# Optimization experiments

Measured on AMD Instinct MI355X. Metric: run time of the kernel, lower is better.

## Reference

```python
import jax, jax.numpy as jnp
import numpy as np

N_NODES = 100000
TIME_LEN = 128
OUT_CH = 5          # temp_out_dim
KERNEL = 7
STRIDE = 3
CONV_OUT_LEN = (TIME_LEN - KERNEL) // STRIDE + 1  # 41
EMB = 32            # temp_emb_dim
HID = EMB // 2      # 16
N_EDGES = 3200000


def setup_inputs() -> dict:
    key = jax.random.key(0)
    ks = jax.random.split(key, 16)
    x = jax.random.normal(ks[0], (N_NODES, TIME_LEN), dtype=jnp.float32)
    edge_index = jax.random.randint(ks[1], (2, N_EDGES), 0, N_NODES, dtype=jnp.int64)
    s = 0.05
    return {
        "x": x,
        "edge_index": edge_index,
        "conv_w": jax.random.normal(ks[2], (OUT_CH, 1, KERNEL), dtype=jnp.float32) * s,
        "conv_b": jax.random.normal(ks[3], (OUT_CH,), dtype=jnp.float32) * s,
        "fc_w": jax.random.normal(ks[4], (EMB, OUT_CH * CONV_OUT_LEN), dtype=jnp.float32) * s,
        "fc_b": jax.random.normal(ks[5], (EMB,), dtype=jnp.float32) * s,
        "g1w1": jax.random.normal(ks[6], (HID, EMB), dtype=jnp.float32) * s,
        "g1b1": jax.random.normal(ks[7], (HID,), dtype=jnp.float32) * s,
        "g1w2": jax.random.normal(ks[8], (HID, HID), dtype=jnp.float32) * s,
        "g1b2": jax.random.normal(ks[9], (HID,), dtype=jnp.float32) * s,
        "g2w1": jax.random.normal(ks[10], (HID, HID), dtype=jnp.float32) * s,
        "g2b1": jax.random.normal(ks[11], (HID,), dtype=jnp.float32) * s,
        "g2w2": jax.random.normal(ks[12], (HID, HID), dtype=jnp.float32) * s,
        "g2b2": jax.random.normal(ks[13], (HID,), dtype=jnp.float32) * s,
        "ro_w": jax.random.normal(ks[14], (1, HID), dtype=jnp.float32) * s,
        "ro_b": jax.random.normal(ks[15], (1,), dtype=jnp.float32) * s,
    }


def _gin_conv(h, edge_index, w1, b1, w2, b2):
    # sum-aggregate neighbor features into target nodes (eps = 0)
    agg = jax.ops.segment_sum(h[edge_index[0]], edge_index[1], num_segments=N_NODES)
    z = h + agg
    # MLP: Linear -> ReLU -> Linear
    return jax.nn.relu(z @ w1.T + b1) @ w2.T + b2


def reference(x, edge_index, conv_w, conv_b, fc_w, fc_b,
              g1w1, g1b1, g1w2, g1b2, g2w1, g2b1, g2w2, g2b2, ro_w, ro_b):
    n = x.shape[0]
    # temporal Conv1d: [N,1,T] -> [N,OUT_CH,CONV_OUT_LEN]
    h = jax.lax.conv_general_dilated(
        x[:, None, :], conv_w, window_strides=(STRIDE,), padding='VALID',
        dimension_numbers=('NCH', 'OIH', 'NCH'))
    h = jax.nn.relu(h + conv_b[None, :, None])
    h = h.reshape(n, -1)                 # channel-major flatten, matches torch .view
    h = h @ fc_w.T + fc_b                # [N, EMB]
    # GIN layer 1 (+ ReLU between layers)
    h = jax.nn.relu(_gin_conv(h, edge_index, g1w1, g1b1, g1w2, g1b2))
    # GIN layer 2 (no activation after final layer)
    h = _gin_conv(h, edge_index, g2w1, g2b1, g2w2, g2b2)
    return h @ ro_w.T + ro_b             # [N, 1]
```

## Files before the change

kernel.cpp:

```cpp
#include <hip/hip_runtime.h>

#define NN   100000
#define TL   128
#define OC   5
#define KW   7
#define ST   3
#define CL   41
#define FLAT 205
#define EMB  32
#define HID  16
#define NE   3200000

#define CLP  44
#define JP   220
#define JB   55
#define WN   8
#define SXW  1048

#define BBUCK  391
#define NPB    14336
#define TILE   4096
#define NBIN   782
#define CNODES 64
#define NGB    1563
#define NS     2560
#define SENT   0xFFFFFFFFu

__device__ __forceinline__ void f4add(float4& a, const float4 v) {
    a.x += v.x; a.y += v.y; a.z += v.z; a.w += v.w;
}

__global__ __launch_bounds__(256) void k_prep(
    const float* __restrict__ g1w1, const float* __restrict__ fc_w,
    const float* __restrict__ fc_b,
    float* __restrict__ wcTl, float* __restrict__ bc,
    int* __restrict__ gcur)
{
    int tid = threadIdx.x;
    for (int idx = tid; idx < HID * JP; idx += 256) {
        int l  = idx / JP;
        int jp = idx - l * JP;
        int c  = jp / CLP;
        int t  = jp - c * CLP;
        float s = 0.f;
        if (t < CL) {
            int j = c * CL + t;
            #pragma unroll
            for (int m = 0; m < EMB; ++m)
                s = fmaf(g1w1[l * EMB + m], fc_w[m * FLAT + j], s);
        }
        wcTl[idx] = s;
    }
    if (tid < HID) {
        float s = 0.f;
        #pragma unroll
        for (int m = 0; m < EMB; ++m)
            s = fmaf(g1w1[tid * EMB + m], fc_b[m], s);
        bc[tid] = s;
    }
    for (int b = tid; b < BBUCK; b += 256)
        gcur[b] = b * NPB;
}

__global__ __launch_bounds__(256) void k_convfc(
    const float* __restrict__ x,
    const float* __restrict__ conv_w, const float* __restrict__ conv_b,
    const float* __restrict__ wcTl,  const float* __restrict__ bc,
    float* __restrict__ p1)
{
    __shared__ float s_x[4 * SXW];
    __shared__ float s_h2[4 * WN * JP];
    const int tid  = threadIdx.x;
    const int wv   = tid >> 6;
    const int lane = tid & 63;
    const long long nw = (long long)blockIdx.x * 32 + wv * WN;

    float* sx = s_x  + wv * SXW;
    float* sh = s_h2 + wv * (WN * JP);

    const float4* xv = (const float4*)(x + nw * TL);
    #pragma unroll
    for (int c = 0; c < 4; ++c) {
        int f4  = c * 64 + lane;
        int row = f4 >> 5;
        int c4  = f4 & 31;
        float4 v = xv[f4];
        float* d = sx + row * 129 + c4 * 4;
        d[0] = v.x; d[1] = v.y; d[2] = v.z; d[3] = v.w;
    }
    asm volatile("s_waitcnt lgkmcnt(0)" ::: "memory");

    for (int i = lane; i < 55 * WN; i += 64) {
        int n  = i & (WN - 1);
        int ci = i >> 3;
        int c  = ci / 11;
        int tg = ci - c * 11;
        int t0 = tg * 4;
        const float* xr = sx + n * 129 + t0 * ST;
        float xx[16];
        #pragma unroll
        for (int k = 0; k < 16; ++k) xx[k] = xr[k];
        const float* wr = conv_w + c * KW;
        float w0 = wr[0], w1 = wr[1], w2 = wr[2], w3 = wr[3],
              w4 = wr[4], w5 = wr[5], w6 = wr[6];
        float bb = conv_b[c];
        float4 r;
        r.x = fmaxf(bb + xx[0]*w0 + xx[1]*w1 + xx[2]*w2 + xx[3]*w3
                       + xx[4]*w4 + xx[5]*w5 + xx[6]*w6, 0.f);
        r.y = (t0 + 1 < CL)
            ? fmaxf(bb + xx[3]*w0 + xx[4]*w1 + xx[5]*w2 + xx[6]*w3
                       + xx[7]*w4 + xx[8]*w5 + xx[9]*w6, 0.f) : 0.f;
        r.z = (t0 + 2 < CL)
            ? fmaxf(bb + xx[6]*w0 + xx[7]*w1 + xx[8]*w2 + xx[9]*w3
                       + xx[10]*w4 + xx[11]*w5 + xx[12]*w6, 0.f) : 0.f;
        r.w = (t0 + 3 < CL)
            ? fmaxf(bb + xx[9]*w0 + xx[10]*w1 + xx[11]*w2 + xx[12]*w3
                       + xx[13]*w4 + xx[14]*w5 + xx[15]*w6, 0.f) : 0.f;
        *(float4*)(sh + n * JP + c * CLP + t0) = r;
    }
    asm volatile("s_waitcnt lgkmcnt(0)" ::: "memory");

    const int l = lane & 15;
    const int g = lane >> 4;
    float a0 = bc[l];
    float a1 = a0;
    const float4* wl = (const float4*)(wcTl + l * JP);
    const float4* h0 = (const float4*)(sh + g * JP);
    const float4* h1 = (const float4*)(sh + (g + 4) * JP);
    #pragma unroll 5
    for (int jb = 0; jb < JB; ++jb) {
        float4 w = wl[jb];
        float4 p = h0[jb];
        float4 q = h1[jb];
        a0 = fmaf(p.x, w.x, fmaf(p.y, w.y, fmaf(p.z, w.z, fmaf(p.w, w.w, a0))));
        a1 = fmaf(q.x, w.x, fmaf(q.y, w.y, fmaf(q.z, w.z, fmaf(q.w, w.w, a1))));
    }
    p1[(nw + g)     * HID + l] = a0;
    p1[(nw + g + 4) * HID + l] = a1;
}

__global__ __launch_bounds__(256) void k_bin(
    const int* __restrict__ ei, int* __restrict__ gcur,
    unsigned int* __restrict__ gbin)
{
    __shared__ unsigned int s_stage[TILE];
    __shared__ int s_cnt[BBUCK], s_ofs[BBUCK], s_base[BBUCK];
    __shared__ int s_sum[256];

    const int tid = threadIdx.x;
    const int e0  = blockIdx.x * TILE;
    const int cntE = min(TILE, NE - e0);

    for (int b = tid; b < BBUCK; b += 256) s_cnt[b] = 0;
    __syncthreads();

    for (int i = tid; i < cntE; i += 256)
        atomicAdd(&s_cnt[ei[NE + e0 + i] >> 8], 1);
    __syncthreads();

    for (int b = tid; b < BBUCK; b += 256) {
        int c = s_cnt[b];
        s_base[b] = c ? atomicAdd(&gcur[b], (c + 15) & ~15) : 0;
    }

    int v0 = 0, v1 = 0;
    {
        int i0 = tid * 2;
        if (i0     < BBUCK) v0 = s_cnt[i0];
        if (i0 + 1 < BBUCK) v1 = s_cnt[i0 + 1];
    }
    int csum = v0 + v1;
    s_sum[tid] = csum;
    __syncthreads();
    #pragma unroll
    for (int d = 1; d < 256; d <<= 1) {
        int t = (tid >= d) ? s_sum[tid - d] : 0;
        __syncthreads();
        s_sum[tid] += t;
        __syncthreads();
    }
    {
        int run = s_sum[tid] - csum;
        int i0 = tid * 2;
        if (i0     < BBUCK) { s_ofs[i0]     = run; run += v0; }
        if (i0 + 1 < BBUCK) { s_ofs[i0 + 1] = run; }
    }
    __syncthreads();

    for (int i = tid; i < cntE; i += 256) {
        int s = ei[e0 + i];
        int d = ei[NE + e0 + i];
        int b = d >> 8;
        int pos = atomicAdd(&s_ofs[b], 1);
        s_stage[pos] = ((unsigned int)(d & 255) << 17) | (unsigned int)s;
    }
    __syncthreads();

    const int wid = tid >> 6, lane = tid & 63;
    for (int b = wid; b < BBUCK; b += 4) {
        int cnt = s_cnt[b];
        if (!cnt) continue;
        int res = (cnt + 15) & ~15;
        int rdo = s_ofs[b] - cnt;
        int gb  = s_base[b];
        int lim = min(res, b * NPB + NPB - gb);
        for (int j = lane; j < lim; j += 64)
            gbin[(size_t)gb + j] = (j < cnt) ? s_stage[rdo + j] : SENT;
    }
}

__global__ __launch_bounds__(256) void k_sort(
    const unsigned int* __restrict__ gbin, const int* __restrict__ gcur,
    int* __restrict__ goff, int* __restrict__ gsorted)
{
    __shared__ unsigned int s_m[NS];
    __shared__ int s_cnt[CNODES], s_ofs[CNODES], s_loc[CNODES];
    __shared__ int s_n;
    const int tid = threadIdx.x;
    const int b64 = blockIdx.x;
    const int bkt = b64 >> 2, q = b64 & 3;
    const int nslots = min(gcur[bkt] - bkt * NPB, NPB);
    const unsigned int* run = gbin + (size_t)bkt * NPB;

    if (tid < CNODES) s_cnt[tid] = 0;
    if (tid == 0) s_n = 0;
    __syncthreads();

    for (int i = tid; i < nslots; i += 256) {
        unsigned int w = run[i];
        if (w != SENT && (int)(w >> 23) == q) {
            int p = atomicAdd(&s_n, 1);
            if (p < NS) {
                s_m[p] = w;
                atomicAdd(&s_cnt[(w >> 17) & 63], 1);
            }
        }
    }
    __syncthreads();

    if (tid < CNODES) s_ofs[tid] = s_cnt[tid];
    __syncthreads();
    #pragma unroll
    for (int d = 1; d < CNODES; d <<= 1) {
        int t = (tid < CNODES && tid >= d) ? s_ofs[tid - d] : 0;
        __syncthreads();
        if (tid < CNODES) s_ofs[tid] += t;
        __syncthreads();
    }
    if (tid < CNODES) {
        int inc = s_ofs[tid];
        s_loc[tid] = inc - s_cnt[tid];
        goff[(size_t)b64 * 65 + tid + 1] = inc;
    }
    if (tid == 0) goff[(size_t)b64 * 65] = 0;
    __syncthreads();

    const int n = min(s_n, NS);
    int* dst = gsorted + (size_t)b64 * NS;
    for (int i = tid; i < n; i += 256) {
        unsigned int w = s_m[i];
        int pos = atomicAdd(&s_loc[(w >> 17) & 63], 1);
        dst[pos] = (int)(w & 0x1FFFFu);
    }
}

__global__ __launch_bounds__(256) void k_gagg1(
    const float* __restrict__ feat, const int* __restrict__ goff,
    const int* __restrict__ gsorted,
    const float* __restrict__ b1, const float* __restrict__ w2,
    const float* __restrict__ b2, const float* __restrict__ w3,
    float* __restrict__ outfeat)
{
    __shared__ float s_acc[CNODES * 16];
    __shared__ float s_w2[HID * HID], s_w3[HID * HID], s_b1[HID], s_b2[HID];
    __shared__ int s_off[CNODES + 1];
    const int tid = threadIdx.x;
    const int b   = blockIdx.x;

    s_w2[tid] = w2[tid];
    s_w3[tid] = w3[tid];
    if (tid < HID) { s_b1[tid] = b1[tid]; s_b2[tid] = b2[tid]; }
    if (tid < CNODES + 1) s_off[tid] = goff[(size_t)b * 65 + tid];
    __syncthreads();

    const int node = tid >> 2, q = tid & 3;
    const int* srcs = gsorted + (size_t)b * NS;
    const float4* pv = (const float4*)feat;
    float4 acc0 = make_float4(0.f, 0.f, 0.f, 0.f);
    float4 acc1 = make_float4(0.f, 0.f, 0.f, 0.f);
    int j = s_off[node];
    const int e = s_off[node + 1];
    for (; j + 7 < e; j += 8) {
        int s0 = srcs[j],     s1 = srcs[j + 1], s2 = srcs[j + 2], s3 = srcs[j + 3];
        int s4 = srcs[j + 4], s5 = srcs[j + 5], s6 = srcs[j + 6], s7 = srcs[j + 7];
        float4 v0 = pv[(size_t)s0 * 4 + q];
        float4 v1 = pv[(size_t)s1 * 4 + q];
        float4 v2 = pv[(size_t)s2 * 4 + q];
        float4 v3 = pv[(size_t)s3 * 4 + q];
        float4 v4 = pv[(size_t)s4 * 4 + q];
        float4 v5 = pv[(size_t)s5 * 4 + q];
        float4 v6 = pv[(size_t)s6 * 4 + q];
        float4 v7 = pv[(size_t)s7 * 4 + q];
        f4add(acc0, v0); f4add(acc1, v1); f4add(acc0, v2); f4add(acc1, v3);
        f4add(acc0, v4); f4add(acc1, v5); f4add(acc0, v6); f4add(acc1, v7);
    }
    for (; j + 3 < e; j += 4) {
        int s0 = srcs[j], s1 = srcs[j + 1], s2 = srcs[j + 2], s3 = srcs[j + 3];
        float4 v0 = pv[(size_t)s0 * 4 + q];
        float4 v1 = pv[(size_t)s1 * 4 + q];
        float4 v2 = pv[(size_t)s2 * 4 + q];
        float4 v3 = pv[(size_t)s3 * 4 + q];
        f4add(acc0, v0); f4add(acc1, v1); f4add(acc0, v2); f4add(acc1, v3);
    }
    for (; j < e; ++j)
        f4add(acc0, pv[(size_t)srcs[j] * 4 + q]);
    f4add(acc0, acc1);
    ((float4*)s_acc)[node * 4 + q] = acc0;
    __syncthreads();

    const int gn = b * CNODES + tid;
    if (tid < CNODES && gn < NN) {
        const float4* fr = (const float4*)(feat + (size_t)gn * HID);
        const float4* sa = (const float4*)(s_acc + tid * 16);
        float t[HID];
        #pragma unroll
        for (int i2 = 0; i2 < 4; ++i2) {
            float4 f = fr[i2], a = sa[i2];
            t[i2*4+0] = fmaxf(f.x + a.x + s_b1[i2*4+0], 0.f);
            t[i2*4+1] = fmaxf(f.y + a.y + s_b1[i2*4+1], 0.f);
            t[i2*4+2] = fmaxf(f.z + a.z + s_b1[i2*4+2], 0.f);
            t[i2*4+3] = fmaxf(f.w + a.w + s_b1[i2*4+3], 0.f);
        }
        float h[HID];
        #pragma unroll
        for (int i2 = 0; i2 < HID; ++i2) {
            float acc = s_b2[i2];
            #pragma unroll
            for (int jj = 0; jj < HID; ++jj) acc += t[jj] * s_w2[i2 * HID + jj];
            h[i2] = fmaxf(acc, 0.f);
        }
        float o[HID];
        #pragma unroll
        for (int i2 = 0; i2 < HID; ++i2) {
            float acc = 0.f;
            #pragma unroll
            for (int jj = 0; jj < HID; ++jj) acc += h[jj] * s_w3[i2 * HID + jj];
            o[i2] = acc;
        }
        float4* po = (float4*)(outfeat + (size_t)gn * HID);
        #pragma unroll
        for (int i2 = 0; i2 < 4; ++i2)
            po[i2] = make_float4(o[i2*4+0], o[i2*4+1], o[i2*4+2], o[i2*4+3]);
    }
}

__global__ __launch_bounds__(256) void k_gagg2(
    const float* __restrict__ feat, const int* __restrict__ goff,
    const int* __restrict__ gsorted,
    const float* __restrict__ b1, const float* __restrict__ w2,
    const float* __restrict__ b2, const float* __restrict__ row,
    const float* __restrict__ rob,
    float* __restrict__ out)
{
    __shared__ float s_acc[CNODES * 16];
    __shared__ float s_w2[HID * HID], s_b1[HID], s_b2[HID], s_ro[HID];
    __shared__ int s_off[CNODES + 1];
    const int tid = threadIdx.x;
    const int b   = blockIdx.x;

    s_w2[tid] = w2[tid];
    if (tid < HID) { s_b1[tid] = b1[tid]; s_b2[tid] = b2[tid]; s_ro[tid] = row[tid]; }
    if (tid < CNODES + 1) s_off[tid] = goff[(size_t)b * 65 + tid];
    __syncthreads();

    const int node = tid >> 2, q = tid & 3;
    const int* srcs = gsorted + (size_t)b * NS;
    const float4* pv = (const float4*)feat;
    float4 acc0 = make_float4(0.f, 0.f, 0.f, 0.f);
    float4 acc1 = make_float4(0.f, 0.f, 0.f, 0.f);
    int j = s_off[node];
    const int e = s_off[node + 1];
    for (; j + 7 < e; j += 8) {
        int s0 = srcs[j],     s1 = srcs[j + 1], s2 = srcs[j + 2], s3 = srcs[j + 3];
        int s4 = srcs[j + 4], s5 = srcs[j + 5], s6 = srcs[j + 6], s7 = srcs[j + 7];
        float4 v0 = pv[(size_t)s0 * 4 + q];
        float4 v1 = pv[(size_t)s1 * 4 + q];
        float4 v2 = pv[(size_t)s2 * 4 + q];
        float4 v3 = pv[(size_t)s3 * 4 + q];
        float4 v4 = pv[(size_t)s4 * 4 + q];
        float4 v5 = pv[(size_t)s5 * 4 + q];
        float4 v6 = pv[(size_t)s6 * 4 + q];
        float4 v7 = pv[(size_t)s7 * 4 + q];
        f4add(acc0, v0); f4add(acc1, v1); f4add(acc0, v2); f4add(acc1, v3);
        f4add(acc0, v4); f4add(acc1, v5); f4add(acc0, v6); f4add(acc1, v7);
    }
    for (; j + 3 < e; j += 4) {
        int s0 = srcs[j], s1 = srcs[j + 1], s2 = srcs[j + 2], s3 = srcs[j + 3];
        float4 v0 = pv[(size_t)s0 * 4 + q];
        float4 v1 = pv[(size_t)s1 * 4 + q];
        float4 v2 = pv[(size_t)s2 * 4 + q];
        float4 v3 = pv[(size_t)s3 * 4 + q];
        f4add(acc0, v0); f4add(acc1, v1); f4add(acc0, v2); f4add(acc1, v3);
    }
    for (; j < e; ++j)
        f4add(acc0, pv[(size_t)srcs[j] * 4 + q]);
    f4add(acc0, acc1);
    ((float4*)s_acc)[node * 4 + q] = acc0;
    __syncthreads();

    const int gn = b * CNODES + tid;
    if (tid < CNODES && gn < NN) {
        const float4* fr = (const float4*)(feat + (size_t)gn * HID);
        const float4* sa = (const float4*)(s_acc + tid * 16);
        float t[HID];
        #pragma unroll
        for (int i2 = 0; i2 < 4; ++i2) {
            float4 f = fr[i2], a = sa[i2];
            t[i2*4+0] = fmaxf(f.x + a.x + s_b1[i2*4+0], 0.f);
            t[i2*4+1] = fmaxf(f.y + a.y + s_b1[i2*4+1], 0.f);
            t[i2*4+2] = fmaxf(f.z + a.z + s_b1[i2*4+2], 0.f);
            t[i2*4+3] = fmaxf(f.w + a.w + s_b1[i2*4+3], 0.f);
        }
        float res = rob[0];
        #pragma unroll
        for (int i2 = 0; i2 < HID; ++i2) {
            float acc = s_b2[i2];
            #pragma unroll
            for (int jj = 0; jj < HID; ++jj) acc += t[jj] * s_w2[i2 * HID + jj];
            res += acc * s_ro[i2];
        }
        out[gn] = res;
    }
}

__global__ __launch_bounds__(256) void k_embed(
    const float* __restrict__ x,
    const float* __restrict__ conv_w, const float* __restrict__ conv_b,
    const float* __restrict__ fc_w,   const float* __restrict__ fc_b,
    const float* __restrict__ g1w1,
    float* __restrict__ p1)
{
    __shared__ float s_x[4][TL];
    __shared__ float s_h[4][FLAT + 3];
    __shared__ float s_e[4][EMB];

    const int w    = threadIdx.x >> 6;
    const int lane = threadIdx.x & 63;
    const int node = blockIdx.x * 4 + w;

    const float2* xr = (const float2*)(x + (size_t)node * TL);
    float2 v = xr[lane];
    s_x[w][lane * 2 + 0] = v.x;
    s_x[w][lane * 2 + 1] = v.y;
    __syncthreads();

    for (int o = lane; o < FLAT; o += 64) {
        int c = o / CL;
        int t = o - c * CL;
        float acc = conv_b[c];
        #pragma unroll
        for (int k = 0; k < KW; ++k)
            acc += s_x[w][t * ST + k] * conv_w[c * KW + k];
        s_h[w][o] = fmaxf(acc, 0.f);
    }
    __syncthreads();

    if (lane < EMB) {
        float acc = fc_b[lane];
        const float* wr = fc_w + lane * FLAT;
        for (int j = 0; j < FLAT; ++j)
            acc += s_h[w][j] * wr[j];
        s_e[w][lane] = acc;
    }
    __syncthreads();

    if (lane < HID) {
        float acc = 0.f;
        const float* wr = g1w1 + lane * EMB;
        #pragma unroll
        for (int j = 0; j < EMB; ++j)
            acc += s_e[w][j] * wr[j];
        p1[(size_t)node * HID + lane] = acc;
    }
}

__global__ __launch_bounds__(256) void k_scatter(
    const float* __restrict__ p, const int* __restrict__ ei,
    float* __restrict__ agg)
{
    long long t = (long long)blockIdx.x * 256 + threadIdx.x;
    int e = (int)(t >> 4);
    int k = (int)(t & 15);
    if (e >= NE) return;
    int src = ei[e];
    int dst = ei[NE + e];
    float v = p[(size_t)src * HID + k];
    atomicAdd(agg + (size_t)dst * HID + k, v);
}

__global__ __launch_bounds__(256) void k_mlp1(
    const float* __restrict__ p1, const float* __restrict__ agg,
    const float* __restrict__ b1, const float* __restrict__ w2,
    const float* __restrict__ b2, const float* __restrict__ w3,
    float* __restrict__ p2)
{
    __shared__ float s_w2[HID * HID], s_w3[HID * HID], s_b1[HID], s_b2[HID];
    int tid = threadIdx.x;
    s_w2[tid] = w2[tid];
    s_w3[tid] = w3[tid];
    if (tid < HID) { s_b1[tid] = b1[tid]; s_b2[tid] = b2[tid]; }
    __syncthreads();

    int n = blockIdx.x * 256 + tid;
    if (n >= NN) return;

    float t[HID], h[HID];
    const float4* pa = (const float4*)(p1  + (size_t)n * HID);
    const float4* pb = (const float4*)(agg + (size_t)n * HID);
    #pragma unroll
    for (int i = 0; i < 4; ++i) {
        float4 a = pa[i], b = pb[i];
        t[i*4+0] = fmaxf(a.x + b.x + s_b1[i*4+0], 0.f);
        t[i*4+1] = fmaxf(a.y + b.y + s_b1[i*4+1], 0.f);
        t[i*4+2] = fmaxf(a.z + b.z + s_b1[i*4+2], 0.f);
        t[i*4+3] = fmaxf(a.w + b.w + s_b1[i*4+3], 0.f);
    }
    #pragma unroll
    for (int i = 0; i < HID; ++i) {
        float acc = s_b2[i];
        #pragma unroll
        for (int j = 0; j < HID; ++j) acc += t[j] * s_w2[i * HID + j];
        h[i] = fmaxf(acc, 0.f);
    }
    float o[HID];
    #pragma unroll
    for (int i = 0; i < HID; ++i) {
        float acc = 0.f;
        #pragma unroll
        for (int j = 0; j < HID; ++j) acc += h[j] * s_w3[i * HID + j];
        o[i] = acc;
    }
    float4* po = (float4*)(p2 + (size_t)n * HID);
    #pragma unroll
    for (int i = 0; i < 4; ++i)
        po[i] = make_float4(o[i*4+0], o[i*4+1], o[i*4+2], o[i*4+3]);
}

__global__ __launch_bounds__(256) void k_final(
    const float* __restrict__ p2, const float* __restrict__ agg2,
    const float* __restrict__ b1, const float* __restrict__ w2,
    const float* __restrict__ b2, const float* __restrict__ row,
    const float* __restrict__ rob,
    float* __restrict__ out)
{
    __shared__ float s_w2[HID * HID], s_b1[HID], s_b2[HID], s_ro[HID];
    int tid = threadIdx.x;
    s_w2[tid] = w2[tid];
    if (tid < HID) { s_b1[tid] = b1[tid]; s_b2[tid] = b2[tid]; s_ro[tid] = row[tid]; }
    __syncthreads();

    int n = blockIdx.x * 256 + tid;
    if (n >= NN) return;

    float t[HID];
    const float4* pa = (const float4*)(p2   + (size_t)n * HID);
    const float4* pb = (const float4*)(agg2 + (size_t)n * HID);
    #pragma unroll
    for (int i = 0; i < 4; ++i) {
        float4 a = pa[i], b = pb[i];
        t[i*4+0] = fmaxf(a.x + b.x + s_b1[i*4+0], 0.f);
        t[i*4+1] = fmaxf(a.y + b.y + s_b1[i*4+1], 0.f);
        t[i*4+2] = fmaxf(a.z + b.z + s_b1[i*4+2], 0.f);
        t[i*4+3] = fmaxf(a.w + b.w + s_b1[i*4+3], 0.f);
    }
    float res = rob[0];
    #pragma unroll
    for (int i = 0; i < HID; ++i) {
        float acc = s_b2[i];
        #pragma unroll
        for (int j = 0; j < HID; ++j) acc += t[j] * s_w2[i * HID + j];
        res += acc * s_ro[i];
    }
    out[n] = res;
}

extern "C" void kernel_launch(void* const* d_in, const int* in_sizes, int n_in,
                              void* d_out, int out_size, void* d_ws, size_t ws_size,
                              hipStream_t stream)
{
    const float* x      = (const float*)d_in[0];
    const int*   ei     = (const int*)  d_in[1];
    const float* conv_w = (const float*)d_in[2];
    const float* conv_b = (const float*)d_in[3];
    const float* fc_w   = (const float*)d_in[4];
    const float* fc_b   = (const float*)d_in[5];
    const float* g1w1   = (const float*)d_in[6];
    const float* g1b1   = (const float*)d_in[7];
    const float* g1w2   = (const float*)d_in[8];
    const float* g1b2   = (const float*)d_in[9];
    const float* g2w1   = (const float*)d_in[10];
    const float* g2b1   = (const float*)d_in[11];
    const float* g2w2   = (const float*)d_in[12];
    const float* g2b2   = (const float*)d_in[13];
    const float* ro_w   = (const float*)d_in[14];
    const float* ro_b   = (const float*)d_in[15];
    float* out = (float*)d_out;

    float* A    = (float*)d_ws;
    float* B    = A + (size_t)NN * HID;
    float* wcTl = B + (size_t)NN * HID;
    float* bc   = wcTl + (size_t)HID * JP;
    int*   gcur = (int*)(bc + 16);
    unsigned int* gbin = (unsigned int*)(gcur + BBUCK);
    int*   goff    = (int*)(gbin + (size_t)BBUCK * NPB);
    int*   gsorted = goff + (size_t)NGB * 65;
    const size_t need = (size_t)((char*)(gsorted + (size_t)NGB * NS) - (char*)d_ws);

    if (ws_size >= need) {
        k_prep<<<1, 256, 0, stream>>>(g1w1, fc_w, fc_b, wcTl, bc, gcur);
        k_convfc<<<NN / 32, 256, 0, stream>>>(x, conv_w, conv_b, wcTl, bc, A);
        k_bin<<<NBIN, 256, 0, stream>>>(ei, gcur, gbin);
        k_sort<<<NGB, 256, 0, stream>>>(gbin, gcur, goff, gsorted);
        k_gagg1<<<NGB, 256, 0, stream>>>(A, goff, gsorted, g1b1, g1w2, g1b2,
                                         g2w1, B);
        k_gagg2<<<NGB, 256, 0, stream>>>(B, goff, gsorted, g2b1, g2w2, g2b2,
                                         ro_w, ro_b, out);
    } else {
        k_embed<<<NN / 4, 256, 0, stream>>>(x, conv_w, conv_b, fc_w, fc_b,
                                            g1w1, A);
        hipMemsetAsync(B, 0, (size_t)NN * HID * sizeof(float), stream);
        k_scatter<<<(int)(((long long)NE * HID) / 256), 256, 0, stream>>>(A, ei, B);
        k_mlp1<<<(NN + 255) / 256, 256, 0, stream>>>(A, B, g1b1, g1w2, g1b2,
                                                     g2w1, A);
        hipMemsetAsync(B, 0, (size_t)NN * HID * sizeof(float), stream);
        k_scatter<<<(int)(((long long)NE * HID) / 256), 256, 0, stream>>>(A, ei, B);
        k_final<<<(NN + 255) / 256, 256, 0, stream>>>(A, B, g2b1, g2w2, g2b2,
                                                      ro_w, ro_b, out);
    }
}
```

Baseline: 362.4 us.

## Merge conv/FC embedding and edge binning into one heterogeneous kernel launch

Fuses the independent conv+FC embedding kernel and the edge-binning kernel into a single launch where every fifth block does edge binning and the other four do conv/FC work on node tiles. Shared memory becomes one union buffer sized for the larger role. This lets the compute-heavy embedding and the memory/atomic-heavy binning run concurrently on the GPU and removes one launch boundary. The cost is that every block reserves the larger shared-memory footprint, which may lower occupancy, and the interleaved block schedule can cause imbalance.

After: 363.7 us. About the same (+0.4%).

```diff
diff --git a/kernel.cpp b/kernel.cpp
--- a/kernel.cpp
+++ b/kernel.cpp
@@ -16,15 +16,19 @@
 #define JB   55
 #define WN   8
 #define SXW  1048
+#define NCVB 3125
 
 #define BBUCK  391
 #define NPB    14336
 #define TILE   4096
 #define NBIN   782
+#define CVBG   3910
 #define CNODES 64
 #define NGB    1563
 #define NS     2560
 #define SENT   0xFFFFFFFFu
+
+#define SMEMF  11232
 
 __device__ __forceinline__ void f4add(float4& a, const float4 v) {
     a.x += v.x; a.y += v.y; a.z += v.z; a.w += v.w;
@@ -62,18 +66,96 @@
         gcur[b] = b * NPB;
 }
 
-__global__ __launch_bounds__(256) void k_convfc(
+__global__ __launch_bounds__(256) void k_convbin(
     const float* __restrict__ x,
     const float* __restrict__ conv_w, const float* __restrict__ conv_b,
     const float* __restrict__ wcTl,  const float* __restrict__ bc,
-    float* __restrict__ p1)
-{
-    __shared__ float s_x[4 * SXW];
-    __shared__ float s_h2[4 * WN * JP];
-    const int tid  = threadIdx.x;
+    float* __restrict__ p1,
+    const int* __restrict__ ei, int* __restrict__ gcur,
+    unsigned int* __restrict__ gbin)
+{
+    __shared__ float smem[SMEMF];
+    const int bid = blockIdx.x;
+    const int grp = bid / 5, pos = bid - grp * 5;
+    const int tid = threadIdx.x;
+
+    if (pos == 4) {
+        unsigned int* s_stage = (unsigned int*)smem;
+        int* s_cnt  = (int*)smem + TILE;
+        int* s_ofs  = s_cnt  + BBUCK;
+        int* s_base = s_ofs  + BBUCK;
+        int* s_sum  = s_base + BBUCK;
+
+        const int e0   = grp * TILE;
+        const int cntE = min(TILE, NE - e0);
+
+        for (int b = tid; b < BBUCK; b += 256) s_cnt[b] = 0;
+        __syncthreads();
+
+        for (int i = tid; i < cntE; i += 256)
+            atomicAdd(&s_cnt[ei[NE + e0 + i] >> 8], 1);
+        __syncthreads();
+
+        for (int b = tid; b < BBUCK; b += 256) {
+            int c = s_cnt[b];
+            s_base[b] = c ? atomicAdd(&gcur[b], (c + 15) & ~15) : 0;
+        }
+
+        int v0 = 0, v1 = 0;
+        {
+            int i0 = tid * 2;
+            if (i0     < BBUCK) v0 = s_cnt[i0];
+            if (i0 + 1 < BBUCK) v1 = s_cnt[i0 + 1];
+        }
+        int csum = v0 + v1;
+        s_sum[tid] = csum;
+        __syncthreads();
+        #pragma unroll
+        for (int d = 1; d < 256; d <<= 1) {
+            int t = (tid >= d) ? s_sum[tid - d] : 0;
+            __syncthreads();
+            s_sum[tid] += t;
+            __syncthreads();
+        }
+        {
+            int run = s_sum[tid] - csum;
+            int i0 = tid * 2;
+            if (i0     < BBUCK) { s_ofs[i0]     = run; run += v0; }
+            if (i0 + 1 < BBUCK) { s_ofs[i0 + 1] = run; }
+        }
+        __syncthreads();
+
+        for (int i = tid; i < cntE; i += 256) {
+            int s = ei[e0 + i];
+            int d = ei[NE + e0 + i];
+            int b = d >> 8;
+            int pp = atomicAdd(&s_ofs[b], 1);
+            s_stage[pp] = ((unsigned int)(d & 255) << 17) | (unsigned int)s;
+        }
+        __syncthreads();
+
+        const int wid = tid >> 6, lane = tid & 63;
+        for (int b = wid; b < BBUCK; b += 4) {
+            int cnt = s_cnt[b];
+            if (!cnt) continue;
+            int res = (cnt + 15) & ~15;
+            int rdo = s_ofs[b] - cnt;
+            int gb  = s_base[b];
+            int lim = min(res, b * NPB + NPB - gb);
+            for (int j = lane; j < lim; j += 64)
+                gbin[(size_t)gb + j] = (j < cnt) ? s_stage[rdo + j] : SENT;
+        }
+        return;
+    }
+
+    const int cb = grp * 4 + pos;
+    if (cb >= NCVB) return;
+
+    float* s_x  = smem;
+    float* s_h2 = smem + 4 * SXW;
     const int wv   = tid >> 6;
     const int lane = tid & 63;
-    const long long nw = (long long)blockIdx.x * 32 + wv * WN;
+    const long long nw = (long long)cb * 32 + wv * WN;
 
     float* sx = s_x  + wv * SXW;
     float* sh = s_h2 + wv * (WN * JP);
@@ -137,76 +219,6 @@
     }
     p1[(nw + g)     * HID + l] = a0;
     p1[(nw + g + 4) * HID + l] = a1;
-}
-
-__global__ __launch_bounds__(256) void k_bin(
-    const int* __restrict__ ei, int* __restrict__ gcur,
-    unsigned int* __restrict__ gbin)
-{
-    __shared__ unsigned int s_stage[TILE];
-    __shared__ int s_cnt[BBUCK], s_ofs[BBUCK], s_base[BBUCK];
-    __shared__ int s_sum[256];
-
-    const int tid = threadIdx.x;
-    const int e0  = blockIdx.x * TILE;
-    const int cntE = min(TILE, NE - e0);
-
-    for (int b = tid; b < BBUCK; b += 256) s_cnt[b] = 0;
-    __syncthreads();
-
-    for (int i = tid; i < cntE; i += 256)
-        atomicAdd(&s_cnt[ei[NE + e0 + i] >> 8], 1);
-    __syncthreads();
-
-    for (int b = tid; b < BBUCK; b += 256) {
-        int c = s_cnt[b];
-        s_base[b] = c ? atomicAdd(&gcur[b], (c + 15) & ~15) : 0;
-    }
-
-    int v0 = 0, v1 = 0;
-    {
-        int i0 = tid * 2;
-        if (i0     < BBUCK) v0 = s_cnt[i0];
-        if (i0 + 1 < BBUCK) v1 = s_cnt[i0 + 1];
-    }
-    int csum = v0 + v1;
-    s_sum[tid] = csum;
-    __syncthreads();
-    #pragma unroll
-    for (int d = 1; d < 256; d <<= 1) {
-        int t = (tid >= d) ? s_sum[tid - d] : 0;
-        __syncthreads();
-        s_sum[tid] += t;
-        __syncthreads();
-    }
-    {
-        int run = s_sum[tid] - csum;
-        int i0 = tid * 2;
-        if (i0     < BBUCK) { s_ofs[i0]     = run; run += v0; }
-        if (i0 + 1 < BBUCK) { s_ofs[i0 + 1] = run; }
-    }
-    __syncthreads();
-
-    for (int i = tid; i < cntE; i += 256) {
-        int s = ei[e0 + i];
-        int d = ei[NE + e0 + i];
-        int b = d >> 8;
-        int pos = atomicAdd(&s_ofs[b], 1);
-        s_stage[pos] = ((unsigned int)(d & 255) << 17) | (unsigned int)s;
-    }
-    __syncthreads();
-
-    const int wid = tid >> 6, lane = tid & 63;
-    for (int b = wid; b < BBUCK; b += 4) {
-        int cnt = s_cnt[b];
-        if (!cnt) continue;
-        int res = (cnt + 15) & ~15;
-        int rdo = s_ofs[b] - cnt;
-        int gb  = s_base[b];
-        int lim = min(res, b * NPB + NPB - gb);
-        for (int j = lane; j < lim; j += 64)
-            gbin[(size_t)gb + j] = (j < cnt) ? s_stage[rdo + j] : SENT;
-    }
 }
 
 __global__ __launch_bounds__(256) void k_sort(
@@ -618,8 +630,8 @@
 
     if (ws_size >= need) {
         k_prep<<<1, 256, 0, stream>>>(g1w1, fc_w, fc_b, wcTl, bc, gcur);
-        k_convfc<<<NN / 32, 256, 0, stream>>>(x, conv_w, conv_b, wcTl, bc, A);
-        k_bin<<<NBIN, 256, 0, stream>>>(ei, gcur, gbin);
+        k_convbin<<<CVBG, 256, 0, stream>>>(x, conv_w, conv_b, wcTl, bc, A,
+                                            ei, gcur, gbin);
         k_sort<<<NGB, 256, 0, stream>>>(gbin, gcur, goff, gsorted);
         k_gagg1<<<NGB, 256, 0, stream>>>(A, goff, gsorted, g1b1, g1w2, g1b2,
                                          g2w1, B);
```

## Fuse per-block edge sort into first GIN aggregation kernel; parallelize prep

Applied to the files above, without the earlier changes.

Merges the counting-sort kernel with the first GIN aggregation. The sorted source indices stay in shared memory and are read from there during the gather, while still being written to global memory for the second layer. This removes one kernel launch and a global round trip of the sorted indices and offsets. Separately, the weight-folding prep kernel now runs on 8 blocks instead of 1. Shared memory per block grows (an extra 2560-int array), which may lower occupancy for the latency-bound gather.

New measurement: 349.8 us. 3.5% less time.

```diff
diff --git a/kernel.cpp b/kernel.cpp
--- a/kernel.cpp
+++ b/kernel.cpp
@@ -36,8 +36,9 @@
     float* __restrict__ wcTl, float* __restrict__ bc,
     int* __restrict__ gcur)
 {
-    int tid = threadIdx.x;
-    for (int idx = tid; idx < HID * JP; idx += 256) {
+    const int gid = blockIdx.x * 256 + threadIdx.x;
+    const int gs  = gridDim.x * 256;
+    for (int idx = gid; idx < HID * JP; idx += gs) {
         int l  = idx / JP;
         int jp = idx - l * JP;
         int c  = jp / CLP;
@@ -51,14 +52,14 @@
         }
         wcTl[idx] = s;
     }
-    if (tid < HID) {
+    if (gid < HID) {
         float s = 0.f;
         #pragma unroll
         for (int m = 0; m < EMB; ++m)
-            s = fmaf(g1w1[tid * EMB + m], fc_b[m], s);
-        bc[tid] = s;
-    }
-    for (int b = tid; b < BBUCK; b += 256)
+            s = fmaf(g1w1[gid * EMB + m], fc_b[m], s);
+        bc[gid] = s;
+    }
+    for (int b = gid; b < BBUCK; b += gs)
         gcur[b] = b * NPB;
 }
 
@@ -209,26 +210,37 @@
     }
 }
 
-__global__ __launch_bounds__(256) void k_sort(
+__global__ __launch_bounds__(256) void k_sgagg1(
     const unsigned int* __restrict__ gbin, const int* __restrict__ gcur,
-    int* __restrict__ goff, int* __restrict__ gsorted)
+    const float* __restrict__ feat,
+    const float* __restrict__ b1, const float* __restrict__ w2,
+    const float* __restrict__ b2, const float* __restrict__ w3,
+    int* __restrict__ goff, int* __restrict__ gsorted,
+    float* __restrict__ outfeat)
 {
     __shared__ unsigned int s_m[NS];
-    __shared__ int s_cnt[CNODES], s_ofs[CNODES], s_loc[CNODES];
+    __shared__ int s_sorted[NS];
+    __shared__ float s_acc[CNODES * 16];
+    __shared__ float s_w2[HID * HID], s_w3[HID * HID], s_b1[HID], s_b2[HID];
+    __shared__ int s_cnt[CNODES], s_scan[CNODES], s_loc[CNODES];
+    __shared__ int s_ofx[CNODES + 1];
     __shared__ int s_n;
     const int tid = threadIdx.x;
     const int b64 = blockIdx.x;
-    const int bkt = b64 >> 2, q = b64 & 3;
+    const int bkt = b64 >> 2, qp = b64 & 3;
     const int nslots = min(gcur[bkt] - bkt * NPB, NPB);
     const unsigned int* run = gbin + (size_t)bkt * NPB;
 
+    s_w2[tid] = w2[tid];
+    s_w3[tid] = w3[tid];
+    if (tid < HID) { s_b1[tid] = b1[tid]; s_b2[tid] = b2[tid]; }
     if (tid < CNODES) s_cnt[tid] = 0;
     if (tid == 0) s_n = 0;
     __syncthreads();
 
     for (int i = tid; i < nslots; i += 256) {
         unsigned int w = run[i];
-        if (w != SENT && (int)(w >> 23) == q) {
+        if (w != SENT && (int)(w >> 23) == qp) {
             int p = atomicAdd(&s_n, 1);
             if (p < NS) {
                 s_m[p] = w;
@@ -238,48 +250,124 @@
     }
     __syncthreads();
 
-    if (tid < CNODES) s_ofs[tid] = s_cnt[tid];
+    if (tid < CNODES) s_scan[tid] = s_cnt[tid];
     __syncthreads();
     #pragma unroll
     for (int d = 1; d < CNODES; d <<= 1) {
-        int t = (tid < CNODES && tid >= d) ? s_ofs[tid - d] : 0;
+        int t = (tid < CNODES && tid >= d) ? s_scan[tid - d] : 0;
         __syncthreads();
-        if (tid < CNODES) s_ofs[tid] += t;
+        if (tid < CNODES) s_scan[tid] += t;
         __syncthreads();
     }
     if (tid < CNODES) {
-        int inc = s_ofs[tid];
-        s_loc[tid] = inc - s_cnt[tid];
+        int inc = min(s_scan[tid], NS);
+        s_loc[tid] = inc - min(s_cnt[tid], NS);
+        s_ofx[tid + 1] = inc;
         goff[(size_t)b64 * 65 + tid + 1] = inc;
     }
-    if (tid == 0) goff[(size_t)b64 * 65] = 0;
+    if (tid == 0) { s_ofx[0] = 0; goff[(size_t)b64 * 65] = 0; }
     __syncthreads();
 
     const int n = min(s_n, NS);
-    int* dst = gsorted + (size_t)b64 * NS;
     for (int i = tid; i < n; i += 256) {
         unsigned int w = s_m[i];
         int pos = atomicAdd(&s_loc[(w >> 17) & 63], 1);
-        dst[pos] = (int)(w & 0x1FFFFu);
-    }
-}
-
-__global__ __launch_bounds__(256) void k_gagg1(
+        if (pos < NS) s_sorted[pos] = (int)(w & 0x1FFFFu);
+    }
+    __syncthreads();
+
+    int* gdst = gsorted + (size_t)b64 * NS;
+    for (int i = tid; i < n; i += 256) gdst[i] = s_sorted[i];
+
+    const int node = tid >> 2, q4 = tid & 3;
+    const float4* pv = (const float4*)feat;
+    float4 acc0 = make_float4(0.f, 0.f, 0.f, 0.f);
+    float4 acc1 = make_float4(0.f, 0.f, 0.f, 0.f);
+    int j = s_ofx[node];
+    const int e = s_ofx[node + 1];
+    for (; j + 7 < e; j += 8) {
+        int s0 = s_sorted[j],     s1 = s_sorted[j + 1];
+        int s2 = s_sorted[j + 2], s3 = s_sorted[j + 3];
+        int s4 = s_sorted[j + 4], s5 = s_sorted[j + 5];
+        int s6 = s_sorted[j + 6], s7 = s_sorted[j + 7];
+        float4 v0 = pv[(size_t)s0 * 4 + q4];
+        float4 v1 = pv[(size_t)s1 * 4 + q4];
+        float4 v2 = pv[(size_t)s2 * 4 + q4];
+        float4 v3 = pv[(size_t)s3 * 4 + q4];
+        float4 v4 = pv[(size_t)s4 * 4 + q4];
+        float4 v5 = pv[(size_t)s5 * 4 + q4];
+        float4 v6 = pv[(size_t)s6 * 4 + q4];
+        float4 v7 = pv[(size_t)s7 * 4 + q4];
+        f4add(acc0, v0); f4add(acc1, v1); f4add(acc0, v2); f4add(acc1, v3);
+        f4add(acc0, v4); f4add(acc1, v5); f4add(acc0, v6); f4add(acc1, v7);
+    }
+    for (; j + 3 < e; j += 4) {
+        int s0 = s_sorted[j],     s1 = s_sorted[j + 1];
+        int s2 = s_sorted[j + 2], s3 = s_sorted[j + 3];
+        float4 v0 = pv[(size_t)s0 * 4 + q4];
+        float4 v1 = pv[(size_t)s1 * 4 + q4];
+        float4 v2 = pv[(size_t)s2 * 4 + q4];
+        float4 v3 = pv[(size_t)s3 * 4 + q4];
+        f4add(acc0, v0); f4add(acc1, v1); f4add(acc0, v2); f4add(acc1, v3);
+    }
+    for (; j < e; ++j)
+        f4add(acc0, pv[(size_t)s_sorted[j] * 4 + q4]);
+    f4add(acc0, acc1);
+    ((float4*)s_acc)[node * 4 + q4] = acc0;
+    __syncthreads();
+
+    const int gn = b64 * CNODES + tid;
+    if (tid < CNODES && gn < NN) {
+        const float4* fr = (const float4*)(feat + (size_t)gn * HID);
+        const float4* sa = (const float4*)(s_acc + tid * 16);
+        float t[HID];
+        #pragma unroll
+        for (int i2 = 0; i2 < 4; ++i2) {
+            float4 f = fr[i2], a = sa[i2];
+            t[i2*4+0] = fmaxf(f.x + a.x + s_b1[i2*4+0], 0.f);
+            t[i2*4+1] = fmaxf(f.y + a.y + s_b1[i2*4+1], 0.f);
+            t[i2*4+2] = fmaxf(f.z + a.z + s_b1[i2*4+2], 0.f);
+            t[i2*4+3] = fmaxf(f.w + a.w + s_b1[i2*4+3], 0.f);
+        }
+        float h[HID];
+        #pragma unroll
+        for (int i2 = 0; i2 < HID; ++i2) {
+            float acc = s_b2[i2];
+            #pragma unroll
+            for (int jj = 0; jj < HID; ++jj) acc += t[jj] * s_w2[i2 * HID + jj];
+            h[i2] = fmaxf(acc, 0.f);
+        }
+        float o[HID];
+        #pragma unroll
+        for (int i2 = 0; i2 < HID; ++i2) {
+            float acc = 0.f;
+            #pragma unroll
+            for (int jj = 0; jj < HID; ++jj) acc += h[jj] * s_w3[i2 * HID + jj];
+            o[i2] = acc;
+        }
+        float4* po = (float4*)(outfeat + (size_t)gn * HID);
+        #pragma unroll
+        for (int i2 = 0; i2 < 4; ++i2)
+            po[i2] = make_float4(o[i2*4+0], o[i2*4+1], o[i2*4+2], o[i2*4+3]);
+    }
+}
+
+__global__ __launch_bounds__(256) void k_gagg2(
     const float* __restrict__ feat, const int* __restrict__ goff,
     const int* __restrict__ gsorted,
     const float* __restrict__ b1, const float* __restrict__ w2,
-    const float* __restrict__ b2, const float* __restrict__ w3,
-    float* __restrict__ outfeat)
+    const float* __restrict__ b2, const float* __restrict__ row,
+    const float* __restrict__ rob,
+    float* __restrict__ out)
 {
     __shared__ float s_acc[CNODES * 16];
-    __shared__ float s_w2[HID * HID], s_w3[HID * HID], s_b1[HID], s_b2[HID];
+    __shared__ float s_w2[HID * HID], s_b1[HID], s_b2[HID], s_ro[HID];
     __shared__ int s_off[CNODES + 1];
     const int tid = threadIdx.x;
     const int b   = blockIdx.x;
 
     s_w2[tid] = w2[tid];
-    s_w3[tid] = w3[tid];
-    if (tid < HID) { s_b1[tid] = b1[tid]; s_b2[tid] = b2[tid]; }
+    if (tid < HID) { s_b1[tid] = b1[tid]; s_b2[tid] = b2[tid]; s_ro[tid] = row[tid]; }
     if (tid < CNODES + 1) s_off[tid] = goff[(size_t)b * 65 + tid];
     __syncthreads();
 
@@ -331,96 +419,6 @@
             t[i2*4+2] = fmaxf(f.z + a.z + s_b1[i2*4+2], 0.f);
             t[i2*4+3] = fmaxf(f.w + a.w + s_b1[i2*4+3], 0.f);
         }
-        float h[HID];
-        #pragma unroll
-        for (int i2 = 0; i2 < HID; ++i2) {
-            float acc = s_b2[i2];
-            #pragma unroll
-            for (int jj = 0; jj < HID; ++jj) acc += t[jj] * s_w2[i2 * HID + jj];
-            h[i2] = fmaxf(acc, 0.f);
-        }
-        float o[HID];
-        #pragma unroll
-        for (int i2 = 0; i2 < HID; ++i2) {
-            float acc = 0.f;
-            #pragma unroll
-            for (int jj = 0; jj < HID; ++jj) acc += h[jj] * s_w3[i2 * HID + jj];
-            o[i2] = acc;
-        }
-        float4* po = (float4*)(outfeat + (size_t)gn * HID);
-        #pragma unroll
-        for (int i2 = 0; i2 < 4; ++i2)
-            po[i2] = make_float4(o[i2*4+0], o[i2*4+1], o[i2*4+2], o[i2*4+3]);
-    }
-}
-
-__global__ __launch_bounds__(256) void k_gagg2(
-    const float* __restrict__ feat, const int* __restrict__ goff,
-    const int* __restrict__ gsorted,
-    const float* __restrict__ b1, const float* __restrict__ w2,
-    const float* __restrict__ b2, const float* __restrict__ row,
-    const float* __restrict__ rob,
-    float* __restrict__ out)
-{
-    __shared__ float s_acc[CNODES * 16];
-    __shared__ float s_w2[HID * HID], s_b1[HID], s_b2[HID], s_ro[HID];
-    __shared__ int s_off[CNODES + 1];
-    const int tid = threadIdx.x;
-    const int b   = blockIdx.x;
-
-    s_w2[tid] = w2[tid];
-    if (tid < HID) { s_b1[tid] = b1[tid]; s_b2[tid] = b2[tid]; s_ro[tid] = row[tid]; }
-    if (tid < CNODES + 1) s_off[tid] = goff[(size_t)b * 65 + tid];
-    __syncthreads();
-
-    const int node = tid >> 2, q = tid & 3;
-    const int* srcs = gsorted + (size_t)b * NS;
-    const float4* pv = (const float4*)feat;
-    float4 acc0 = make_float4(0.f, 0.f, 0.f, 0.f);
-    float4 acc1 = make_float4(0.f, 0.f, 0.f, 0.f);
-    int j = s_off[node];
-    const int e = s_off[node + 1];
-    for (; j + 7 < e; j += 8) {
-        int s0 = srcs[j],     s1 = srcs[j + 1], s2 = srcs[j + 2], s3 = srcs[j + 3];
-        int s4 = srcs[j + 4], s5 = srcs[j + 5], s6 = srcs[j + 6], s7 = srcs[j + 7];
-        float4 v0 = pv[(size_t)s0 * 4 + q];
-        float4 v1 = pv[(size_t)s1 * 4 + q];
-        float4 v2 = pv[(size_t)s2 * 4 + q];
-        float4 v3 = pv[(size_t)s3 * 4 + q];
-        float4 v4 = pv[(size_t)s4 * 4 + q];
-        float4 v5 = pv[(size_t)s5 * 4 + q];
-        float4 v6 = pv[(size_t)s6 * 4 + q];
-        float4 v7 = pv[(size_t)s7 * 4 + q];
-        f4add(acc0, v0); f4add(acc1, v1); f4add(acc0, v2); f4add(acc1, v3);
-        f4add(acc0, v4); f4add(acc1, v5); f4add(acc0, v6); f4add(acc1, v7);
-    }
-    for (; j + 3 < e; j += 4) {
-        int s0 = srcs[j], s1 = srcs[j + 1], s2 = srcs[j + 2], s3 = srcs[j + 3];
-        float4 v0 = pv[(size_t)s0 * 4 + q];
-        float4 v1 = pv[(size_t)s1 * 4 + q];
-        float4 v2 = pv[(size_t)s2 * 4 + q];
-        float4 v3 = pv[(size_t)s3 * 4 + q];
-        f4add(acc0, v0); f4add(acc1, v1); f4add(acc0, v2); f4add(acc1, v3);
-    }
-    for (; j < e; ++j)
-        f4add(acc0, pv[(size_t)srcs[j] * 4 + q]);
-    f4add(acc0, acc1);
-    ((float4*)s_acc)[node * 4 + q] = acc0;
-    __syncthreads();
-
-    const int gn = b * CNODES + tid;
-    if (tid < CNODES && gn < NN) {
-        const float4* fr = (const float4*)(feat + (size_t)gn * HID);
-        const float4* sa = (const float4*)(s_acc + tid * 16);
-        float t[HID];
-        #pragma unroll
-        for (int i2 = 0; i2 < 4; ++i2) {
-            float4 f = fr[i2], a = sa[i2];
-            t[i2*4+0] = fmaxf(f.x + a.x + s_b1[i2*4+0], 0.f);
-            t[i2*4+1] = fmaxf(f.y + a.y + s_b1[i2*4+1], 0.f);
-            t[i2*4+2] = fmaxf(f.z + a.z + s_b1[i2*4+2], 0.f);
-            t[i2*4+3] = fmaxf(f.w + a.w + s_b1[i2*4+3], 0.f);
-        }
         float res = rob[0];
         #pragma unroll
         for (int i2 = 0; i2 < HID; ++i2) {
@@ -617,12 +615,11 @@
     const size_t need = (size_t)((char*)(gsorted + (size_t)NGB * NS) - (char*)d_ws);
 
     if (ws_size >= need) {
-        k_prep<<<1, 256, 0, stream>>>(g1w1, fc_w, fc_b, wcTl, bc, gcur);
+        k_prep<<<8, 256, 0, stream>>>(g1w1, fc_w, fc_b, wcTl, bc, gcur);
         k_convfc<<<NN / 32, 256, 0, stream>>>(x, conv_w, conv_b, wcTl, bc, A);
         k_bin<<<NBIN, 256, 0, stream>>>(ei, gcur, gbin);
-        k_sort<<<NGB, 256, 0, stream>>>(gbin, gcur, goff, gsorted);
-        k_gagg1<<<NGB, 256, 0, stream>>>(A, goff, gsorted, g1b1, g1w2, g1b2,
-                                         g2w1, B);
+        k_sgagg1<<<NGB, 256, 0, stream>>>(gbin, gcur, A, g1b1, g1w2, g1b2,
+                                          g2w1, goff, gsorted, B);
         k_gagg2<<<NGB, 256, 0, stream>>>(B, goff, gsorted, g2b1, g2w2, g2b2,
                                          ro_w, ro_b, out);
     } else {
```
